# Kernel optimization log

Hardware: AMD Instinct MI355X
Metric: run time of the kernel (lower is better)

The kernel has to match this reference:

```python
import jax, jax.numpy as jnp
import numpy as np

N = 50000      # nodes
E = 400000     # edges
DIM = 3        # pseudo-coordinate dim
M = 3          # kernel size per dim (closed B-spline, degree 1)
K = M ** DIM   # 27 basis weights
IN = 32
MID = 32
OUT = 32
EPS = 1e-5


def spline_basis(edge_attr):
    """Degree-1 closed B-spline basis. edge_attr: [E, DIM] in [0,1].
    Returns basis [E, 2^DIM], weight indices [E, 2^DIM] into K."""
    bits = (jnp.arange(2 ** DIM)[:, None] >> jnp.arange(DIM)[None, :]) & 1  # [8, DIM]
    scaled = edge_attr * M                       # closed spline: scale by kernel size
    lo = jnp.floor(scaled)
    frac = scaled - lo                           # [E, DIM]
    b = jnp.where(bits[None].astype(bool), frac[:, None, :], 1.0 - frac[:, None, :])
    basis = jnp.prod(b, axis=-1)                 # [E, 8]
    idx = (lo.astype(jnp.int32)[:, None, :] + bits[None]) % M  # [E, 8, DIM]
    strides = M ** jnp.arange(DIM)               # [1, 3, 9]
    widx = jnp.sum(idx * strides, axis=-1)       # [E, 8] in [0, K)
    return basis, widx


def spline_conv(x, src, dst, basis, widx, W, root, bias):
    """x: [N, in]; W: [K, in, out]; mean aggregation + root weight + bias."""
    x_j = x[src]                                          # gather [E, in]
    upd = basis[:, :, None] * x_j[:, None, :]             # [E, 8, in]
    # scatter-add basis-weighted source features into per-(node, weight-idx) bins
    S = jnp.zeros((N, K, x.shape[1]), x.dtype).at[dst[:, None], widx].add(upd)
    deg = jnp.zeros((N,), x.dtype).at[dst].add(1.0)
    deg = jnp.maximum(deg, 1.0)
    msg = jnp.einsum('nki,kio->no', S, W) / deg[:, None]  # mean over incoming edges
    return msg + x @ root + bias


def batchnorm(h, gamma, beta):
    mu = jnp.mean(h, axis=0)
    var = jnp.var(h, axis=0)  # biased, as in torch BN forward
    return (h - mu) * jax.lax.rsqrt(var + EPS) * gamma + beta


def setup_inputs() -> dict:
    key = jax.random.key(0)
    ks = jax.random.split(key, 16)
    d = {}
    d['x'] = jax.random.normal(ks[0], (N, IN), jnp.float32)
    d['edge_index'] = jax.random.randint(ks[1], (2, E), 0, N, dtype=jnp.int32)
    d['edge_attr'] = jax.random.uniform(ks[2], (E, DIM), dtype=jnp.float32)
    d['pos'] = jax.random.normal(ks[3], (N, DIM), jnp.float32)
    def wscale(fan_in):
        return 1.0 / np.sqrt(fan_in)
    d['W1'] = jax.random.normal(ks[4], (K, IN, MID), jnp.float32) * wscale(IN)
    d['root1'] = jax.random.normal(ks[5], (IN, MID), jnp.float32) * wscale(IN)
    d['b1'] = jnp.zeros((MID,), jnp.float32)
    d['W2'] = jax.random.normal(ks[6], (K, MID, 2 * MID), jnp.float32) * wscale(MID)
    d['root2'] = jax.random.normal(ks[7], (MID, 2 * MID), jnp.float32) * wscale(MID)
    d['b2'] = jnp.zeros((2 * MID,), jnp.float32)
    d['gamma'] = jnp.ones((2 * MID,), jnp.float32)
    d['beta'] = jnp.zeros((2 * MID,), jnp.float32)
    c3_in = 2 * MID + 3
    d['W3'] = jax.random.normal(ks[8], (K, c3_in, OUT), jnp.float32) * wscale(c3_in)
    d['root3'] = jax.random.normal(ks[9], (c3_in, OUT), jnp.float32) * wscale(c3_in)
    d['b3'] = jnp.zeros((OUT,), jnp.float32)
    return d


def reference(x, edge_index, edge_attr, pos, W1, root1, b1, W2, root2, b2,
              gamma, beta, W3, root3, b3):
    src, dst = edge_index[0], edge_index[1]
    basis, widx = spline_basis(edge_attr)
    h = jax.nn.elu(spline_conv(x, src, dst, basis, widx, W1, root1, b1))
    h = jax.nn.elu(batchnorm(spline_conv(h, src, dst, basis, widx, W2, root2, b2), gamma, beta))
    h = jnp.concatenate([h, pos], axis=1)
    out = spline_conv(h, src, dst, basis, widx, W3, root3, b3)
    return out
```

## Files before the change

kernel.cpp:

```cpp
#include <hip/hip_runtime.h>
#include <hip/hip_bf16.h>


#define EPS 1e-5f
#define MAXN 50176
#define MAXE 401408
#define SP2 904
#define SP3 2696

typedef __attribute__((ext_vector_type(8))) short short8;
typedef __attribute__((ext_vector_type(4))) float floatx4;

__device__ int             g_deg[MAXN];
__device__ int             g_offs[MAXN + 1];
__device__ int             g_cursor[MAXN];
__device__ int             g_bsum[256];
__device__ uint4           g_emeta[MAXE * 2];
__device__ __align__(16) __hip_bfloat16 g_h0[MAXN * 32];
__device__ __align__(16) __hip_bfloat16 g_h1[MAXN * 32];
__device__ __align__(16) __hip_bfloat16 g_h2[MAXN * 64];
__device__ __align__(16) __hip_bfloat16 g_h3[MAXN * 96];
__device__ __align__(16) __hip_bfloat16 g_Wp1[28672];
__device__ __align__(16) __hip_bfloat16 g_Wp2[57344];
__device__ __align__(16) __hip_bfloat16 g_Wp3[86016];
__device__ float           g_stats[128];
__device__ int             g_isbf16;

__device__ __forceinline__ float loadf(const void* p, int i, bool bf)
{
    return bf ? (float)((const __hip_bfloat16*)p)[i] : ((const float*)p)[i];
}
__device__ __forceinline__ float bf16f(unsigned int u)
{
    return __uint_as_float(u << 16);
}
__device__ __forceinline__ unsigned short bfbits(float f)
{
    union { __hip_bfloat16 h; unsigned short u; } cv;
    cv.h = __float2bfloat16(f);
    return cv.u;
}

__global__ void init_detect(const unsigned int* __restrict__ x, int n)
{
    int i = blockIdx.x * blockDim.x + threadIdx.x;
    if (blockIdx.x == 0 && threadIdx.x < 64) {
        int lane = threadIdx.x;
        int cnt = 0;
        for (int k = lane; k < 256; k += 64) {
            unsigned int lo = x[k] & 0xFFFFu;
            int ex = (int)((lo >> 7) & 0xFFu);
            if (lo == 0u || (ex >= 96 && ex <= 140)) cnt++;
        }
#pragma unroll
        for (int o = 1; o < 64; o <<= 1) cnt += __shfl_xor(cnt, o, 64);
        if (lane == 0) g_isbf16 = (cnt >= 200) ? 1 : 0;
    }
    if (i < n) { g_deg[i] = 0; g_cursor[i] = 0; }
    if (i < 128) g_stats[i] = 0.0f;
}

template <int COUT>
__device__ __forceinline__ void prep_ws_dev(const void* W, const void* root,
                                            __hip_bfloat16* Wp, int t, bool bf)
{
    int j = t & 7;
    int lane = (t >> 3) & 63;
    int rest = t >> 9;
    int kk = rest % 28;
    int nt = rest / 28;
    int k = kk * 32 + (lane >> 4) * 8 + j;
    int o = nt * 16 + (lane & 15);
    float v = (k < 864) ? loadf(W, k * COUT + o, bf)
                        : loadf(root, (k - 864) * COUT + o, bf);
    Wp[t] = __float2bfloat16(v);
}

__device__ __forceinline__ void prep_w3_dev(const void* W, const void* root,
                                            __hip_bfloat16* Wp, int t, bool bf)
{
    const int KB = 84;
    int j = t & 7;
    int lane = (t >> 3) & 63;
    int rest = t >> 9;
    int kk = rest % KB;
    int nt = rest / KB;
    int k = kk * 32 + (lane >> 4) * 8 + j;
    int o = nt * 16 + (lane & 15);
    float v = 0.0f;
    if (k < 2592) {
        int bin = k / 96;
        int ch = k - bin * 96;
        if (ch < 67) v = loadf(W, (bin * 67 + ch) * 32 + o, bf);
    } else {
        int ch = k - 2592;
        if (ch < 67) v = loadf(root, ch * 32 + o, bf);
    }
    Wp[t] = __float2bfloat16(v);
}

__global__ void misc_kernel(const int* __restrict__ dst, const void* __restrict__ x,
                            const void* W1, const void* r1,
                            const void* W2, const void* r2,
                            const void* W3, const void* r3, int E, int N)
{
    int t = blockIdx.x * blockDim.x + threadIdx.x;
    const bool bf = (g_isbf16 != 0);
    if (t < E) { atomicAdd(&g_deg[dst[t]], 1); return; }
    t -= E;
    int nx = N * 32;
    if (t < nx) { g_h0[t] = __float2bfloat16(loadf(x, t, bf)); return; }
    t -= nx;
    if (t < 28672) { prep_ws_dev<32>(W1, r1, g_Wp1, t, bf); return; }
    t -= 28672;
    if (t < 57344) { prep_ws_dev<64>(W2, r2, g_Wp2, t, bf); return; }
    t -= 57344;
    if (t < 86016) { prep_w3_dev(W3, r3, g_Wp3, t, bf); return; }
}

__global__ void scan_blk(int n)
{
    __shared__ int buf[256];
    int tid = threadIdx.x;
    int i = blockIdx.x * 256 + tid;
    int v = (i < n) ? g_deg[i] : 0;
    buf[tid] = v;
    __syncthreads();
    for (int o = 1; o < 256; o <<= 1) {
        int t = (tid >= o) ? buf[tid - o] : 0;
        __syncthreads();
        buf[tid] += t;
        __syncthreads();
    }
    if (i < n) g_offs[i] = buf[tid] - v;
    if (tid == 255) g_bsum[blockIdx.x] = buf[255];
}

__global__ void scan_top(int nb, int n)
{
    __shared__ int buf[256];
    int tid = threadIdx.x;
    int v = (tid < nb) ? g_bsum[tid] : 0;
    buf[tid] = v;
    __syncthreads();
    for (int o = 1; o < 256; o <<= 1) {
        int t = (tid >= o) ? buf[tid - o] : 0;
        __syncthreads();
        buf[tid] += t;
        __syncthreads();
    }
    if (tid < nb) g_bsum[tid] = buf[tid] - v;
    if (tid == nb - 1) g_offs[n] = buf[tid];
}

__global__ void scan_add(int n)
{
    int i = blockIdx.x * 256 + threadIdx.x;
    if (i < n) g_offs[i] += g_bsum[i >> 8];
}

__global__ void basis_fill(const void* __restrict__ attr,
                           const int* __restrict__ src,
                           const int* __restrict__ dst, int E)
{
    int e = blockIdx.x * blockDim.x + threadIdx.x;
    if (e >= E) return;
    const bool bf = (g_isbf16 != 0);
    float f[3];
    int lo[3];
#pragma unroll
    for (int d = 0; d < 3; ++d) {
        float a = loadf(attr, e * 3 + d, bf);
        float s = a * 3.0f;
        float l = floorf(s);
        lo[d] = (int)l;
        f[d] = s - l;
    }
    const int p3[3] = {1, 3, 9};
    unsigned int wxp0 = 0, wxp1 = 0;
    unsigned short bb[8];
#pragma unroll
    for (int b = 0; b < 8; ++b) {
        float w = 1.0f;
        int id = 0;
#pragma unroll
        for (int d = 0; d < 3; ++d) {
            int bit = (b >> d) & 1;
            w *= bit ? f[d] : (1.0f - f[d]);
            id += ((lo[d] + bit) % 3) * p3[d];
        }
        if (b < 4) wxp0 |= (unsigned int)id << (8 * b);
        else       wxp1 |= (unsigned int)id << (8 * (b - 4));
        bb[b] = bfbits(w);
    }
    int d = dst[e];
    int p = atomicAdd(&g_cursor[d], 1);
    int slot = g_offs[d] + p;
    g_emeta[slot * 2] = make_uint4(wxp0, wxp1,
                                   (unsigned int)bb[0] | ((unsigned int)bb[1] << 16),
                                   (unsigned int)bb[2] | ((unsigned int)bb[3] << 16));
    g_emeta[slot * 2 + 1] = make_uint4(
        (unsigned int)bb[4] | ((unsigned int)bb[5] << 16),
        (unsigned int)bb[6] | ((unsigned int)bb[7] << 16),
        (unsigned int)src[e], 0u);
}

template <int COUT, bool ELU, int IN_SEL, int OUT_SEL>
__global__ __launch_bounds__(512, 8) void fused_conv(const void* __restrict__ bias,
                                                     int N)
{
    __shared__ unsigned short Sb[8 * SP2];
    __shared__ uint4 recs[8][64];
    __shared__ float invd[8];
    int tid = threadIdx.x, wid = tid >> 6, lane = tid & 63;
    int nbase = blockIdx.x * 8;
    const bool bf = (g_isbf16 != 0);
    const unsigned short* xptr = (IN_SEL == 0) ? (const unsigned short*)g_h0
                                               : (const unsigned short*)g_h1;
    const __hip_bfloat16* Wp = (COUT == 32) ? g_Wp1 : g_Wp2;

    int n = nbase + wid;
    int m = lane & 15, quad = lane >> 4;

    if (n < N) {
        int e0 = g_offs[n], e1 = g_offs[n + 1];
        floatx4 C00 = {}, C01 = {}, C10 = {}, C11 = {};
        uint4* myrec = &recs[wid][0];
        int bin0 = m, bin1 = m + 16;
        for (int base = e0; base < e1; base += 32) {
            int cnt = e1 - base; if (cnt > 32) cnt = 32;
            if (lane < 32) {
                uint4 v0 = make_uint4(0, 0, 0, 0), v1 = make_uint4(0, 0, 0, 0);
                if (lane < cnt) {
                    size_t le = (size_t)(base + lane) * 2;
                    v0 = g_emeta[le];
                    v1 = g_emeta[le + 1];
                }
                myrec[2 * lane] = v0;
                myrec[2 * lane + 1] = v1;
            }
            __builtin_amdgcn_s_waitcnt(0);
            int jmax = (cnt + 3) >> 2;
            unsigned a0w[4] = {0, 0, 0, 0}, a1w[4] = {0, 0, 0, 0};
            unsigned b0w[4] = {0, 0, 0, 0}, b1w[4] = {0, 0, 0, 0};
#pragma unroll
            for (int j = 0; j < 8; ++j) {
                if (j >= jmax) break;
                int kidx = j * 4 + quad;
                uint4 ra = myrec[2 * kidx];
                uint2 rb = *(const uint2*)&myrec[2 * kidx + 1];
                int sn = (int)((const unsigned*)&myrec[2 * kidx + 1])[2];
                unsigned av0 = xptr[(size_t)sn * 32 + m];
                unsigned av1 = xptr[(size_t)sn * 32 + 16 + m];
                unsigned p0 = 0, p1 = 0;
#pragma unroll
                for (int b = 0; b < 8; ++b) {
                    unsigned wx = ((b < 4 ? ra.x : ra.y) >> (8 * (b & 3))) & 0xFFu;
                    unsigned basw = (b < 2) ? ra.z : (b < 4) ? ra.w
                                  : (b < 6) ? rb.x : rb.y;
                    unsigned bas = (b & 1) ? (basw >> 16) : (basw & 0xFFFFu);
                    if (wx == (unsigned)bin0) p0 = bas;
                    if (wx == (unsigned)bin1) p1 = bas;
                }
                unsigned sh = 16 * (j & 1);
                a0w[j >> 1] |= av0 << sh;
                a1w[j >> 1] |= av1 << sh;
                b0w[j >> 1] |= p0 << sh;
                b1w[j >> 1] |= p1 << sh;
            }
            union U { unsigned w[4]; short8 v; } A0, A1, B0, B1;
#pragma unroll
            for (int q = 0; q < 4; ++q) {
                A0.w[q] = a0w[q]; A1.w[q] = a1w[q];
                B0.w[q] = b0w[q]; B1.w[q] = b1w[q];
            }
            C00 = __builtin_amdgcn_mfma_f32_16x16x32_bf16(A0.v, B0.v, C00, 0, 0, 0);
            C01 = __builtin_amdgcn_mfma_f32_16x16x32_bf16(A0.v, B1.v, C01, 0, 0, 0);
            C10 = __builtin_amdgcn_mfma_f32_16x16x32_bf16(A1.v, B0.v, C10, 0, 0, 0);
            C11 = __builtin_amdgcn_mfma_f32_16x16x32_bf16(A1.v, B1.v, C11, 0, 0, 0);
        }
        unsigned short* Srow = Sb + wid * SP2;
        {
            floatx4 Cf[4] = {C00, C01, C10, C11};
#pragma unroll
            for (int f = 0; f < 4; ++f) {
                int mt = f >> 1, nt = f & 1;
                int bin = nt * 16 + m;
                if (bin < 27) {
                    union { unsigned short h[4]; uint2 u; } pk;
#pragma unroll
                    for (int r = 0; r < 4; ++r) pk.h[r] = bfbits(Cf[f][r]);
                    *(uint2*)(Srow + bin * 32 + mt * 16 + quad * 4) = pk.u;
                }
            }
        }
        if (lane < 32) Srow[864 + lane] = xptr[(size_t)n * 32 + lane];
        if (lane == 0) {
            int deg = e1 - e0;
            invd[wid] = 1.0f / (float)(deg < 1 ? 1 : deg);
        }
    }
    __syncthreads();

    if (wid * 16 < COUT) {
        int mrow = m & 7;
        const unsigned short* Ab = Sb + mrow * SP2 + quad * 8;
        floatx4 accS = {}, accR = {};
#pragma unroll
        for (int kk = 0; kk < 28; ++kk) {
            short8 a = *(const short8*)(Ab + kk * 32);
            const short* bp = (const short*)Wp +
                ((size_t)(wid * 28 + kk) * 64 + lane) * 8;
            short8 b = *(const short8*)bp;
            if (kk < 27) accS = __builtin_amdgcn_mfma_f32_16x16x32_bf16(a, b, accS, 0, 0, 0);
            else         accR = __builtin_amdgcn_mfma_f32_16x16x32_bf16(a, b, accR, 0, 0, 0);
        }
        int o = wid * 16 + m;
        float bval = loadf(bias, o, bf);
#pragma unroll
        for (int r = 0; r < 4; ++r) {
            int slot = quad * 4 + r;
            if (slot >= 8) continue;
            int nn = nbase + slot;
            if (nn >= N) continue;
            float v = accS[r] * invd[slot] + accR[r] + bval;
            if (ELU) v = v > 0.0f ? v : expm1f(v);
            if (OUT_SEL == 1) g_h1[nn * 32 + o] = __float2bfloat16(v);
            else              g_h2[nn * 64 + o] = __float2bfloat16(v);
        }
    }
}

__global__ __launch_bounds__(512, 4) void fused_conv3(const void* __restrict__ bias,
                                                      void* __restrict__ out_ext,
                                                      int N)
{
    __shared__ __align__(16) unsigned short Sb[8 * SP3];
    __shared__ union {
        uint4 recs[8][64];
        float red[6][64][4];
    } u;
    __shared__ float invd[8];
    int tid = threadIdx.x, wid = tid >> 6, lane = tid & 63;
    int nbase = blockIdx.x * 8;
    const bool bf = (g_isbf16 != 0);
    const unsigned short* xptr = (const unsigned short*)g_h3;

    int n = nbase + wid;
    int m = lane & 15, quad = lane >> 4;

    if (n < N) {
        int e0 = g_offs[n], e1 = g_offs[n + 1];
        floatx4 C[6][2];
#pragma unroll
        for (int t = 0; t < 6; ++t) {
            C[t][0] = (floatx4){0.f, 0.f, 0.f, 0.f};
            C[t][1] = (floatx4){0.f, 0.f, 0.f, 0.f};
        }
        uint4* myrec = &u.recs[wid][0];
        int bin0 = m, bin1 = m + 16;
        for (int base = e0; base < e1; base += 32) {
            int cnt = e1 - base; if (cnt > 32) cnt = 32;
            if (lane < 32) {
                uint4 v0 = make_uint4(0, 0, 0, 0), v1 = make_uint4(0, 0, 0, 0);
                if (lane < cnt) {
                    size_t le = (size_t)(base + lane) * 2;
                    v0 = g_emeta[le];
                    v1 = g_emeta[le + 1];
                }
                myrec[2 * lane] = v0;
                myrec[2 * lane + 1] = v1;
            }
            __builtin_amdgcn_s_waitcnt(0);
            int jmax = (cnt + 3) >> 2;
            unsigned aw[6][4] = {{0, 0, 0, 0}, {0, 0, 0, 0}, {0, 0, 0, 0},
                                 {0, 0, 0, 0}, {0, 0, 0, 0}, {0, 0, 0, 0}};
            unsigned b0w[4] = {0, 0, 0, 0}, b1w[4] = {0, 0, 0, 0};
#pragma unroll
            for (int j = 0; j < 8; ++j) {
                if (j >= jmax) break;
                int kidx = j * 4 + quad;
                uint4 ra = myrec[2 * kidx];
                uint2 rb = *(const uint2*)&myrec[2 * kidx + 1];
                int sn = (int)((const unsigned*)&myrec[2 * kidx + 1])[2];
                const unsigned short* hr = xptr + (size_t)sn * 96 + m;
                unsigned av[6];
#pragma unroll
                for (int t = 0; t < 6; ++t) av[t] = hr[t * 16];
                unsigned p0 = 0, p1 = 0;
#pragma unroll
                for (int b = 0; b < 8; ++b) {
                    unsigned wx = ((b < 4 ? ra.x : ra.y) >> (8 * (b & 3))) & 0xFFu;
                    unsigned basw = (b < 2) ? ra.z : (b < 4) ? ra.w
                                  : (b < 6) ? rb.x : rb.y;
                    unsigned bas = (b & 1) ? (basw >> 16) : (basw & 0xFFFFu);
                    if (wx == (unsigned)bin0) p0 = bas;
                    if (wx == (unsigned)bin1) p1 = bas;
                }
                unsigned sh = 16 * (j & 1);
#pragma unroll
                for (int t = 0; t < 6; ++t) aw[t][j >> 1] |= av[t] << sh;
                b0w[j >> 1] |= p0 << sh;
                b1w[j >> 1] |= p1 << sh;
            }
            union U { unsigned w[4]; short8 v; } A, B0, B1;
#pragma unroll
            for (int q = 0; q < 4; ++q) { B0.w[q] = b0w[q]; B1.w[q] = b1w[q]; }
#pragma unroll
            for (int t = 0; t < 6; ++t) {
#pragma unroll
                for (int q = 0; q < 4; ++q) A.w[q] = aw[t][q];
                C[t][0] = __builtin_amdgcn_mfma_f32_16x16x32_bf16(A.v, B0.v, C[t][0], 0, 0, 0);
                C[t][1] = __builtin_amdgcn_mfma_f32_16x16x32_bf16(A.v, B1.v, C[t][1], 0, 0, 0);
            }
        }
        unsigned short* Srow = Sb + wid * SP3;
#pragma unroll
        for (int t = 0; t < 6; ++t) {
#pragma unroll
            for (int ntile = 0; ntile < 2; ++ntile) {
                int bin = ntile * 16 + m;
                if (bin < 27) {
                    union { unsigned short h[4]; uint2 uu; } pk;
#pragma unroll
                    for (int r = 0; r < 4; ++r) pk.h[r] = bfbits(C[t][ntile][r]);
                    *(uint2*)(Srow + bin * 96 + t * 16 + quad * 4) = pk.uu;
                }
            }
        }
        for (int t2 = lane; t2 < 96; t2 += 64)
            Srow[2592 + t2] = xptr[(size_t)n * 96 + t2];
        if (lane == 0) {
            int deg = e1 - e0;
            invd[wid] = 1.0f / (float)(deg < 1 ? 1 : deg);
        }
    }
    __syncthreads();

    int nt = wid & 1, kq = wid >> 1;
    int mrow = m & 7;
    const unsigned short* Ab = Sb + mrow * SP3 + quad * 8;
    floatx4 accS = {}, accR = {};
    {
        int kbeg = kq * 21, kend = kbeg + 21;
        int ksplit = (kend < 81) ? kend : 81;
        for (int kk = kbeg; kk < ksplit; ++kk) {
            short8 a = *(const short8*)(Ab + kk * 32);
            const short* bp = (const short*)g_Wp3 +
                ((size_t)(nt * 84 + kk) * 64 + lane) * 8;
            short8 b = *(const short8*)bp;
            accS = __builtin_amdgcn_mfma_f32_16x16x32_bf16(a, b, accS, 0, 0, 0);
        }
        for (int kk = ksplit; kk < kend; ++kk) {
            short8 a = *(const short8*)(Ab + kk * 32);
            const short* bp = (const short*)g_Wp3 +
                ((size_t)(nt * 84 + kk) * 64 + lane) * 8;
            short8 b = *(const short8*)bp;
            accR = __builtin_amdgcn_mfma_f32_16x16x32_bf16(a, b, accR, 0, 0, 0);
        }
    }
    if (kq < 3)
        *(floatx4*)&u.red[wid][lane][0] = accS;
    __syncthreads();
    if (kq == 3) {
#pragma unroll
        for (int w = 0; w < 3; ++w)
            accS += *(const floatx4*)&u.red[2 * w + nt][lane][0];
        int o = nt * 16 + m;
        float bval = loadf(bias, o, bf);
#pragma unroll
        for (int r = 0; r < 4; ++r) {
            int slot = quad * 4 + r;
            if (slot >= 8) continue;
            int nn = nbase + slot;
            if (nn >= N) continue;
            float v = accS[r] * invd[slot] + accR[r] + bval;
            if (bf) ((__hip_bfloat16*)out_ext)[nn * 32 + o] = __float2bfloat16(v);
            else    ((float*)out_ext)[nn * 32 + o] = v;
        }
    }
}

__global__ void bn_reduce(int n)
{
    int tid = threadIdx.x;
    int c = tid & 63;
    int r = tid >> 6;
    float s = 0.0f, s2 = 0.0f;
    for (int i = blockIdx.x * 4 + r; i < n; i += gridDim.x * 4) {
        float v = (float)g_h2[i * 64 + c];
        s += v; s2 += v * v;
    }
    __shared__ float b1s[256], b2s[256];
    b1s[tid] = s; b2s[tid] = s2;
    __syncthreads();
    if (r == 0) {
        s  = b1s[c] + b1s[c + 64] + b1s[c + 128] + b1s[c + 192];
        s2 = b2s[c] + b2s[c + 64] + b2s[c + 128] + b2s[c + 192];
        atomicAdd(&g_stats[c], s);
        atomicAdd(&g_stats[64 + c], s2);
    }
}

__global__ void h3_build(const void* __restrict__ pos,
                         const void* __restrict__ gamma,
                         const void* __restrict__ beta, int N)
{
    __shared__ float cf[128];
    int t = threadIdx.x;
    const bool bf = (g_isbf16 != 0);
    if (t < 64) {
        float inv_n = 1.0f / (float)N;
        float mu = g_stats[t] * inv_n;
        float var = g_stats[64 + t] * inv_n - mu * mu;
        float A = rsqrtf(var + EPS) * loadf(gamma, t, bf);
        cf[t] = A;
        cf[64 + t] = loadf(beta, t, bf) - mu * A;
    }
    __syncthreads();
    int idx = blockIdx.x * blockDim.x + t;
    if (idx >= N * 96) return;
    int n = idx / 96, ch = idx - n * 96;
    float v;
    if (ch < 64) {
        float h = (float)g_h2[n * 64 + ch];
        v = h * cf[ch] + cf[64 + ch];
        v = v > 0.0f ? v : expm1f(v);
    } else if (ch < 67) {
        v = loadf(pos, n * 3 + (ch - 64), bf);
    } else {
        v = 0.0f;
    }
    g_h3[(size_t)n * 96 + ch] = __float2bfloat16(v);
}

extern "C" void kernel_launch(void* const* d_in, const int* in_sizes, int n_in,
                              void* d_out, int out_size, void* d_ws, size_t ws_size,
                              hipStream_t stream)
{
    const void* x      = d_in[0];
    const int*  eindex = (const int*)d_in[1];
    const void* eattr  = d_in[2];
    const void* pos    = d_in[3];
    const void* W1     = d_in[4];
    const void* root1  = d_in[5];
    const void* b1     = d_in[6];
    const void* W2     = d_in[7];
    const void* root2  = d_in[8];
    const void* b2     = d_in[9];
    const void* gamma  = d_in[10];
    const void* beta   = d_in[11];
    const void* W3     = d_in[12];
    const void* root3  = d_in[13];
    const void* b3     = d_in[14];
    (void)d_ws; (void)ws_size; (void)n_in; (void)out_size;

    const int N = in_sizes[0] / 32;
    const int E = in_sizes[1] / 2;
    const int* srcp = eindex;
    const int* dstp = eindex + E;

    init_detect<<<(N + 255) / 256, 256, 0, stream>>>((const unsigned int*)x, N);
    {
        int tot = E + N * 32 + 28672 + 57344 + 86016;
        misc_kernel<<<(tot + 255) / 256, 256, 0, stream>>>(
            dstp, x, W1, root1, W2, root2, W3, root3, E, N);
    }
    int nb = (N + 255) / 256;
    scan_blk<<<nb, 256, 0, stream>>>(N);
    scan_top<<<1, 256, 0, stream>>>(nb, N);
    scan_add<<<nb, 256, 0, stream>>>(N);
    basis_fill<<<(E + 255) / 256, 256, 0, stream>>>(eattr, srcp, dstp, E);

    int nb8 = (N + 7) / 8;
    fused_conv<32, true, 0, 1><<<nb8, 512, 0, stream>>>(b1, N);
    fused_conv<64, false, 1, 2><<<nb8, 512, 0, stream>>>(b2, N);
    bn_reduce<<<120, 256, 0, stream>>>(N);
    h3_build<<<(N * 96 + 255) / 256, 256, 0, stream>>>(pos, gamma, beta, N);
    fused_conv3<<<nb8, 512, 0, stream>>>(b3, d_out, N);
}
```

Baseline: 379.3 us.

## Precompute dense per-edge basis rows and drop LDS edge-record staging

The basis kernel now expands each edge's 8 (weight-index, basis) pairs into a dense 32-entry bf16 row indexed by weight bin (64 bytes per edge), plus a separate source-index array. The conv kernels then read the basis value for their bin directly from global memory, removing the LDS staging of edge records, the waitcnt, and the per-lane 8-way compare/select loop. In exchange, edge metadata traffic grows from 32 to 68 bytes per edge and is re-read by every conv layer. Each 16-lane group's loads hit one contiguous row, so they should coalesce.

```diff
diff --git a/kernel.cpp b/kernel.cpp
--- a/kernel.cpp
+++ b/kernel.cpp
@@ -15,7 +15,8 @@
 __device__ int             g_offs[MAXN + 1];
 __device__ int             g_cursor[MAXN];
 __device__ int             g_bsum[256];
-__device__ uint4           g_emeta[MAXE * 2];
+__device__ int             g_esrc[MAXE];
+__device__ __align__(16) uint4 g_ebas[MAXE * 4];
 __device__ __align__(16) __hip_bfloat16 g_h0[MAXN * 32];
 __device__ __align__(16) __hip_bfloat16 g_h1[MAXN * 32];
 __device__ __align__(16) __hip_bfloat16 g_h2[MAXN * 64];
@@ -177,7 +178,7 @@
         f[d] = s - l;
     }
     const int p3[3] = {1, 3, 9};
-    unsigned int wxp0 = 0, wxp1 = 0;
+    int wx8[8];
     unsigned short bb[8];
 #pragma unroll
     for (int b = 0; b < 8; ++b) {
@@ -189,20 +190,29 @@
             w *= bit ? f[d] : (1.0f - f[d]);
             id += ((lo[d] + bit) % 3) * p3[d];
         }
-        if (b < 4) wxp0 |= (unsigned int)id << (8 * b);
-        else       wxp1 |= (unsigned int)id << (8 * (b - 4));
+        wx8[b] = id;
         bb[b] = bfbits(w);
+    }
+    unsigned wds[16];
+#pragma unroll
+    for (int i = 0; i < 16; ++i) {
+        unsigned w = 0;
+#pragma unroll
+        for (int b = 0; b < 8; ++b) {
+            if (wx8[b] == 2 * i)     w |= (unsigned)bb[b];
+            if (wx8[b] == 2 * i + 1) w |= (unsigned)bb[b] << 16;
+        }
+        wds[i] = w;
     }
     int d = dst[e];
     int p = atomicAdd(&g_cursor[d], 1);
     int slot = g_offs[d] + p;
-    g_emeta[slot * 2] = make_uint4(wxp0, wxp1,
-                                   (unsigned int)bb[0] | ((unsigned int)bb[1] << 16),
-                                   (unsigned int)bb[2] | ((unsigned int)bb[3] << 16));
-    g_emeta[slot * 2 + 1] = make_uint4(
-        (unsigned int)bb[4] | ((unsigned int)bb[5] << 16),
-        (unsigned int)bb[6] | ((unsigned int)bb[7] << 16),
-        (unsigned int)src[e], 0u);
+    uint4* out4 = &g_ebas[(size_t)slot * 4];
+    out4[0] = make_uint4(wds[0],  wds[1],  wds[2],  wds[3]);
+    out4[1] = make_uint4(wds[4],  wds[5],  wds[6],  wds[7]);
+    out4[2] = make_uint4(wds[8],  wds[9],  wds[10], wds[11]);
+    out4[3] = make_uint4(wds[12], wds[13], wds[14], wds[15]);
+    g_esrc[slot] = src[e];
 }
 
 template <int COUT, bool ELU, int IN_SEL, int OUT_SEL>
@@ -210,7 +220,6 @@
                                                      int N)
 {
     __shared__ unsigned short Sb[8 * SP2];
-    __shared__ uint4 recs[8][64];
     __shared__ float invd[8];
     int tid = threadIdx.x, wid = tid >> 6, lane = tid & 63;
     int nbase = blockIdx.x * 8;
@@ -225,21 +234,8 @@
     if (n < N) {
         int e0 = g_offs[n], e1 = g_offs[n + 1];
         floatx4 C00 = {}, C01 = {}, C10 = {}, C11 = {};
-        uint4* myrec = &recs[wid][0];
-        int bin0 = m, bin1 = m + 16;
         for (int base = e0; base < e1; base += 32) {
             int cnt = e1 - base; if (cnt > 32) cnt = 32;
-            if (lane < 32) {
-                uint4 v0 = make_uint4(0, 0, 0, 0), v1 = make_uint4(0, 0, 0, 0);
-                if (lane < cnt) {
-                    size_t le = (size_t)(base + lane) * 2;
-                    v0 = g_emeta[le];
-                    v1 = g_emeta[le + 1];
-                }
-                myrec[2 * lane] = v0;
-                myrec[2 * lane + 1] = v1;
-            }
-            __builtin_amdgcn_s_waitcnt(0);
             int jmax = (cnt + 3) >> 2;
             unsigned a0w[4] = {0, 0, 0, 0}, a1w[4] = {0, 0, 0, 0};
             unsigned b0w[4] = {0, 0, 0, 0}, b1w[4] = {0, 0, 0, 0};
@@ -247,21 +243,18 @@
             for (int j = 0; j < 8; ++j) {
                 if (j >= jmax) break;
                 int kidx = j * 4 + quad;
-                uint4 ra = myrec[2 * kidx];
-                uint2 rb = *(const uint2*)&myrec[2 * kidx + 1];
-                int sn = (int)((const unsigned*)&myrec[2 * kidx + 1])[2];
+                int e = base + kidx;
+                int sn = 0;
+                unsigned p0 = 0, p1 = 0;
+                if (kidx < cnt) {
+                    sn = g_esrc[e];
+                    const unsigned short* brow =
+                        (const unsigned short*)&g_ebas[(size_t)e * 4];
+                    p0 = brow[m];
+                    p1 = brow[16 + m];
+                }
                 unsigned av0 = xptr[(size_t)sn * 32 + m];
                 unsigned av1 = xptr[(size_t)sn * 32 + 16 + m];
-                unsigned p0 = 0, p1 = 0;
-#pragma unroll
-                for (int b = 0; b < 8; ++b) {
-                    unsigned wx = ((b < 4 ? ra.x : ra.y) >> (8 * (b & 3))) & 0xFFu;
-                    unsigned basw = (b < 2) ? ra.z : (b < 4) ? ra.w
-                                  : (b < 6) ? rb.x : rb.y;
-                    unsigned bas = (b & 1) ? (basw >> 16) : (basw & 0xFFFFu);
-                    if (wx == (unsigned)bin0) p0 = bas;
-                    if (wx == (unsigned)bin1) p1 = bas;
-                }
                 unsigned sh = 16 * (j & 1);
                 a0w[j >> 1] |= av0 << sh;
                 a1w[j >> 1] |= av1 << sh;
@@ -336,10 +329,7 @@
                                                       int N)
 {
     __shared__ __align__(16) unsigned short Sb[8 * SP3];
-    __shared__ union {
-        uint4 recs[8][64];
-        float red[6][64][4];
-    } u;
+    __shared__ float red[6][64][4];
     __shared__ float invd[8];
     int tid = threadIdx.x, wid = tid >> 6, lane = tid & 63;
     int nbase = blockIdx.x * 8;
@@ -357,21 +347,8 @@
             C[t][0] = (floatx4){0.f, 0.f, 0.f, 0.f};
             C[t][1] = (floatx4){0.f, 0.f, 0.f, 0.f};
         }
-        uint4* myrec = &u.recs[wid][0];
-        int bin0 = m, bin1 = m + 16;
         for (int base = e0; base < e1; base += 32) {
             int cnt = e1 - base; if (cnt > 32) cnt = 32;
-            if (lane < 32) {
-                uint4 v0 = make_uint4(0, 0, 0, 0), v1 = make_uint4(0, 0, 0, 0);
-                if (lane < cnt) {
-                    size_t le = (size_t)(base + lane) * 2;
-                    v0 = g_emeta[le];
-                    v1 = g_emeta[le + 1];
-                }
-                myrec[2 * lane] = v0;
-                myrec[2 * lane + 1] = v1;
-            }
-            __builtin_amdgcn_s_waitcnt(0);
             int jmax = (cnt + 3) >> 2;
             unsigned aw[6][4] = {{0, 0, 0, 0}, {0, 0, 0, 0}, {0, 0, 0, 0},
                                  {0, 0, 0, 0}, {0, 0, 0, 0}, {0, 0, 0, 0}};
@@ -380,23 +357,20 @@
             for (int j = 0; j < 8; ++j) {
                 if (j >= jmax) break;
                 int kidx = j * 4 + quad;
-                uint4 ra = myrec[2 * kidx];
-                uint2 rb = *(const uint2*)&myrec[2 * kidx + 1];
-                int sn = (int)((const unsigned*)&myrec[2 * kidx + 1])[2];
+                int e = base + kidx;
+                int sn = 0;
+                unsigned p0 = 0, p1 = 0;
+                if (kidx < cnt) {
+                    sn = g_esrc[e];
+                    const unsigned short* brow =
+                        (const unsigned short*)&g_ebas[(size_t)e * 4];
+                    p0 = brow[m];
+                    p1 = brow[16 + m];
+                }
                 const unsigned short* hr = xptr + (size_t)sn * 96 + m;
                 unsigned av[6];
 #pragma unroll
                 for (int t = 0; t < 6; ++t) av[t] = hr[t * 16];
-                unsigned p0 = 0, p1 = 0;
-#pragma unroll
-                for (int b = 0; b < 8; ++b) {
-                    unsigned wx = ((b < 4 ? ra.x : ra.y) >> (8 * (b & 3))) & 0xFFu;
-                    unsigned basw = (b < 2) ? ra.z : (b < 4) ? ra.w
-                                  : (b < 6) ? rb.x : rb.y;
-                    unsigned bas = (b & 1) ? (basw >> 16) : (basw & 0xFFFFu);
-                    if (wx == (unsigned)bin0) p0 = bas;
-                    if (wx == (unsigned)bin1) p1 = bas;
-                }
                 unsigned sh = 16 * (j & 1);
 #pragma unroll
                 for (int t = 0; t < 6; ++t) aw[t][j >> 1] |= av[t] << sh;
@@ -460,12 +434,12 @@
         }
     }
     if (kq < 3)
-        *(floatx4*)&u.red[wid][lane][0] = accS;
+        *(floatx4*)&red[wid][lane][0] = accS;
     __syncthreads();
     if (kq == 3) {
 #pragma unroll
         for (int w = 0; w < 3; ++w)
-            accS += *(const floatx4*)&u.red[2 * w + nt][lane][0];
+            accS += *(const floatx4*)&red[2 * w + nt][lane][0];
         int o = nt * 16 + m;
         float bval = loadf(bias, o, bf);
 #pragma unroll
```

After: 431.7 us. 13.8% more time.
